# Kernel tuning notes

Measured on AMD Instinct MI355X. Metric: run time of the kernel, lower is better.

Reference implementation:

```python
import jax, jax.numpy as jnp
import numpy as np

H, KVH, HD = 32, 8, 128
DM = 4096
LN_L, LN_R = 64, 64
K_BITS, V_BITS = 4, 4
ROPE_THETA = 10000.0


def _rope(x, pos):
    # x: [B, nH, S, D], pos: [B, S]
    D = x.shape[-1]
    inv_freq = 1.0 / (ROPE_THETA ** (jnp.arange(0, D, 2, dtype=jnp.float32) / D))
    freqs = pos[:, :, None].astype(jnp.float32) * inv_freq            # [B,S,D/2]
    emb = jnp.concatenate([freqs, freqs], axis=-1)                     # [B,S,D]
    cos = jnp.cos(emb)[:, None, :, :]
    sin = jnp.sin(emb)[:, None, :, :]
    x1, x2 = x[..., : D // 2], x[..., D // 2:]
    rot = jnp.concatenate([-x2, x1], axis=-1)
    return x * cos + rot * sin


def _fake_quant(x, bits):
    # per-token (last-dim row) symmetric fake quantization
    qmax = 2.0 ** (bits - 1) - 1.0
    s = jnp.maximum(jnp.max(jnp.abs(x), axis=-1, keepdims=True) / qmax, 1e-8)
    return jnp.clip(jnp.round(x / s), -qmax, qmax) * s


def setup_inputs() -> dict:
    key = jax.random.key(0)
    ks = jax.random.split(key, 10)
    B, S = 1, 2048
    hidden_states = jax.random.normal(ks[0], (B, S, DM), dtype=jnp.float32)
    causal = jnp.tril(jnp.ones((S, S), dtype=bool))
    attention_mask = jnp.where(causal, 0.0, -1e9).astype(jnp.float32)[None, None]  # [1,1,S,S]
    position_ids = jnp.arange(S, dtype=jnp.int32)[None, :]
    sc = 1.0 / np.sqrt(DM)
    Wq = jax.random.normal(ks[1], (DM, H * HD), dtype=jnp.float32) * sc
    Wk = jax.random.normal(ks[2], (DM, KVH * HD), dtype=jnp.float32) * sc
    Wv = jax.random.normal(ks[3], (DM, KVH * HD), dtype=jnp.float32) * sc
    Wo = jax.random.normal(ks[4], (H * HD, DM), dtype=jnp.float32) * (1.0 / np.sqrt(H * HD))
    ln_left = jnp.eye(LN_L, dtype=jnp.float32) + 0.02 * jax.random.normal(ks[5], (LN_L, LN_L), dtype=jnp.float32)
    ln_right = jnp.eye(LN_R, dtype=jnp.float32) + 0.02 * jax.random.normal(ks[6], (LN_R, LN_R), dtype=jnp.float32)
    Tk = jnp.eye(HD, dtype=jnp.float32) + 0.05 * jax.random.normal(ks[7], (HD, HD), dtype=jnp.float32)
    Tv = jnp.eye(HD, dtype=jnp.float32) + 0.05 * jax.random.normal(ks[8], (HD, HD), dtype=jnp.float32)
    return {"hidden_states": hidden_states, "attention_mask": attention_mask,
            "position_ids": position_ids, "ln_left": ln_left, "ln_right": ln_right,
            "Wq": Wq, "Wk": Wk, "Wv": Wv, "Wo": Wo, "Tk": Tk, "Tv": Tv}


def reference(hidden_states, attention_mask, position_ids,
              ln_left, ln_right, Wq, Wk, Wv, Wo, Tk, Tv):
    B, S, _ = hidden_states.shape
    # ln_trans: Kronecker-decomposed SVD transform on hidden dim (64x64)
    h = hidden_states.reshape(B, S, LN_L, LN_R)
    h = jnp.einsum('bslr,la,rc->bsac', h, ln_left, ln_right).reshape(B, S, DM)
    # q/k/v projections (effective, trans-absorbed weights)
    q = (h @ Wq).reshape(B, S, H, HD).transpose(0, 2, 1, 3)    # [B,H,S,hd]
    k = (h @ Wk).reshape(B, S, KVH, HD).transpose(0, 2, 1, 3)  # [B,KVH,S,hd]
    v = ((h @ Wv).reshape(B, S, KVH, HD) @ Tv).transpose(0, 2, 1, 3)  # vcache_trans on V
    # RoPE
    q = _rope(q, position_ids)
    k = _rope(k, position_ids)
    # kcache_trans: q gets inv-transpose, k gets forward transform, then fake-quant K
    Tk_inv_t = jnp.linalg.inv(Tk).T
    q = q @ Tk_inv_t
    k = _fake_quant(k @ Tk, K_BITS)
    # vcache quant
    v = _fake_quant(v, V_BITS)
    # GQA repeat
    rep = H // KVH
    k = jnp.repeat(k, rep, axis=1)
    v = jnp.repeat(v, rep, axis=1)
    scores = jnp.einsum('bhqd,bhkd->bhqk', q, k) / np.sqrt(HD) + attention_mask
    p = jax.nn.softmax(scores.astype(jnp.float32), axis=-1).astype(q.dtype)
    o = jnp.einsum('bhqk,bhkd->bhqd', p, v).transpose(0, 2, 1, 3)  # [B,S,H,hd]
    # undo vcache_trans per head, then output projection
    o = o @ jnp.linalg.inv(Tv)
    return o.reshape(B, S, DM) @ Wo
```

## Files before the change

kernel.cpp:

```cpp
#include <hip/hip_runtime.h>
#include <math.h>

#define S_    2048
#define DM_   4096
#define H_    32
#define KVH_  8
#define HD_   128

typedef __bf16 bf16x8 __attribute__((ext_vector_type(8)));
typedef float  f32x4  __attribute__((ext_vector_type(4)));
typedef unsigned short u16x8 __attribute__((ext_vector_type(8)));
typedef unsigned short ushort_t;

__device__ __forceinline__ ushort_t f2b(float f) {
  unsigned int u = __float_as_uint(f);
  unsigned int r = (u + 0x7fffu + ((u >> 16) & 1u)) >> 16;
  return (ushort_t)r;
}
__device__ __forceinline__ float b2f(ushort_t h) {
  return __uint_as_float(((unsigned int)h) << 16);
}
__device__ __forceinline__ bf16x8 asbf(u16x8 v) {
  return __builtin_bit_cast(bf16x8, v);
}

__device__ __forceinline__ void gload16(const void* g, void* l) {
  __builtin_amdgcn_global_load_lds(
      (const __attribute__((address_space(1))) void*)g,
      (__attribute__((address_space(3))) void*)(unsigned int)(unsigned long long)l,
      16, 0, 0);
}

__global__ void newton_init(const float* __restrict__ A0, const float* __restrict__ A1,
                            float* __restrict__ X0, float* __restrict__ X1)
{
  const float* A = blockIdx.x ? A1 : A0;
  float*       X = blockIdx.x ? X1 : X0;
  const int i = blockIdx.y * 1024 + threadIdx.x;
  const int r = i >> 7, c = i & 127;
  X[i] = ((r == c) ? 2.0f : 0.0f) - A[i];
}

__global__ __launch_bounds__(256) void nmm(
    const float* __restrict__ A0, const float* __restrict__ B0, float* __restrict__ C0, int tr0,
    const float* __restrict__ A1, const float* __restrict__ B1, float* __restrict__ C1, int tr1,
    int update)
{
  const float* A = blockIdx.y ? A1 : A0;
  const float* B = blockIdx.y ? B1 : B0;
  float*       C = blockIdx.y ? C1 : C0;
  const int tr   = blockIdx.y ? tr1 : tr0;
  const int m0   = blockIdx.x * 32;
  const int tid  = threadIdx.x;

  __shared__ float Bs[128][132];
  __shared__ float As[32][132];

#pragma unroll
  for (int i = 0; i < 16; ++i) {
    int idx = tid + i * 256;
    int row = idx >> 5, c4 = (idx & 31) * 4;
    *(float4*)&Bs[row][c4] = *(const float4*)&B[row * 128 + c4];
  }
#pragma unroll
  for (int i = 0; i < 4; ++i) {
    int idx = tid + i * 256;
    int row = idx >> 5, c4 = (idx & 31) * 4;
    *(float4*)&As[row][c4] = *(const float4*)&A[(m0 + row) * 128 + c4];
  }
  __syncthreads();

  const int rloc = tid >> 3;
  const int c0   = (tid & 7) * 16;
  float acc[16];
#pragma unroll
  for (int j = 0; j < 16; ++j) acc[j] = 0.0f;
  for (int k = 0; k < 128; ++k) {
    float a = As[rloc][k];
#pragma unroll
    for (int j = 0; j < 16; j += 4) {
      float4 bv = *(const float4*)&Bs[k][c0 + j];
      acc[j + 0] += a * bv.x; acc[j + 1] += a * bv.y;
      acc[j + 2] += a * bv.z; acc[j + 3] += a * bv.w;
    }
  }
#pragma unroll
  for (int j = 0; j < 16; ++j) {
    float v = update ? (2.0f * As[rloc][c0 + j] - acc[j]) : acc[j];
    if (tr) C[(c0 + j) * 128 + (m0 + rloc)] = v;
    else    C[(m0 + rloc) * 128 + c0 + j]   = v;
  }
}

__global__ void prep_all(const float* __restrict__ Tkit, const float* __restrict__ Tk,
                         const float* __restrict__ Tv,   const float* __restrict__ TvI,
                         const float* __restrict__ lnR,  const float* __restrict__ lnL,
                         ushort_t* __restrict__ Fhi, ushort_t* __restrict__ Flo,
                         ushort_t* __restrict__ RBh, ushort_t* __restrict__ RBl,
                         ushort_t* __restrict__ LBh, ushort_t* __restrict__ LBl)
{
  const int mat = blockIdx.x;
  const int t   = threadIdx.x;
  if (mat < 4) {
    const float* src = (mat == 0) ? Tkit : ((mat == 1) ? Tk : ((mat == 2) ? Tv : TvI));
    const int tr = (mat == 3);
    ushort_t* hi = Fhi + mat * 16384;
    ushort_t* lo = Flo + mat * 16384;
    for (int ch = 0; ch < 32; ++ch) {
      int nt = ch >> 2, ds = ch & 3;
#pragma unroll
      for (int i = 0; i < 2; ++i) {
        int idx = t + i * 256;
        int ln = idx >> 3, j = idx & 7;
        int cc = ln & 15, gg = ln >> 4;
        int d = ds * 32 + gg * 8 + j, n = nt * 16 + cc;
        float x = tr ? src[n * 128 + d] : src[d * 128 + n];
        ushort_t hb = f2b(x);
        hi[(ch << 9) + idx] = hb;
        lo[(ch << 9) + idx] = f2b(x - b2f(hb));
      }
    }
  } else {
    const float* src = (mat == 4) ? lnR : lnL;
    ushort_t* hp = (mat == 4) ? RBh : LBh;
    ushort_t* lp = (mat == 4) ? RBl : LBl;
    for (int ch = 0; ch < 8; ++ch) {
      int nt = ch >> 1, ds = ch & 1;
#pragma unroll
      for (int i = 0; i < 2; ++i) {
        int idx = t + i * 256;
        int ln = idx >> 3, j = idx & 7;
        int cc = ln & 15, gg = ln >> 4;
        float x = src[(ds * 32 + gg * 8 + j) * 64 + nt * 16 + cc];
        ushort_t hb = f2b(x);
        hp[(ch << 9) + idx] = hb;
        lp[(ch << 9) + idx] = f2b(x - b2f(hb));
      }
    }
  }
}

__global__ void rope_table(const int* __restrict__ pos,
                           float* __restrict__ cosT, float* __restrict__ sinT)
{
  const int s = blockIdx.x, i = threadIdx.x;
  float invf = 1.0f / (float)pow(10000.0, (double)i * (1.0 / 64.0));
  float ang  = (float)pos[s] * invf;
  cosT[s * 64 + i] = cosf(ang);
  sinT[s * 64 + i] = sinf(ang);
}

__global__ __launch_bounds__(256) void ln3(
    const float* __restrict__ hid,
    const ushort_t* __restrict__ RBh, const ushort_t* __restrict__ RBl,
    const ushort_t* __restrict__ LBh, const ushort_t* __restrict__ LBl,
    ushort_t* __restrict__ hb16, ushort_t* __restrict__ hlo16)
{
  const int blk = blockIdx.x;
  const int tid = threadIdx.x;
  const int w = tid >> 6, lane = tid & 63;
  const int c = lane & 15, g = lane >> 4;

  __shared__ float Hs[4][64 * 68];

#pragma unroll
  for (int i = 0; i < 16; ++i) {
    int idx = tid + i * 256;
    int t = idx >> 10, e = idx & 1023;
    int l = e >> 4, r4 = (e & 15) * 4;
    *(float4*)&Hs[t][l * 68 + r4] =
        *(const float4*)&hid[((size_t)(blk * 4 + t)) * 4096 + l * 64 + r4];
  }
  __syncthreads();

  float* Hw = Hs[w];

  u16x8 ah[4][2], al[4][2];
#pragma unroll
  for (int mt = 0; mt < 4; ++mt)
#pragma unroll
    for (int ds = 0; ds < 2; ++ds) {
      u16x8 th, tl;
#pragma unroll
      for (int j = 0; j < 8; ++j) {
        float x = Hw[(mt * 16 + c) * 68 + ds * 32 + g * 8 + j];
        ushort_t hb = f2b(x); th[j] = hb; tl[j] = f2b(x - b2f(hb));
      }
      ah[mt][ds] = th; al[mt][ds] = tl;
    }

  f32x4 acc[4][4];
#pragma unroll
  for (int mt = 0; mt < 4; ++mt)
#pragma unroll
    for (int nt = 0; nt < 4; ++nt) acc[mt][nt] = (f32x4){0.f, 0.f, 0.f, 0.f};
#pragma unroll
  for (int nt = 0; nt < 4; ++nt) {
    u16x8 bh[2], bl[2];
#pragma unroll
    for (int ds = 0; ds < 2; ++ds) {
      bh[ds] = *(const u16x8*)(RBh + ((nt * 2 + ds) << 9) + lane * 8);
      bl[ds] = *(const u16x8*)(RBl + ((nt * 2 + ds) << 9) + lane * 8);
    }
#pragma unroll
    for (int mt = 0; mt < 4; ++mt)
#pragma unroll
      for (int ds = 0; ds < 2; ++ds) {
        acc[mt][nt] = __builtin_amdgcn_mfma_f32_16x16x32_bf16(asbf(ah[mt][ds]), asbf(bh[ds]), acc[mt][nt], 0, 0, 0);
        acc[mt][nt] = __builtin_amdgcn_mfma_f32_16x16x32_bf16(asbf(ah[mt][ds]), asbf(bl[ds]), acc[mt][nt], 0, 0, 0);
        acc[mt][nt] = __builtin_amdgcn_mfma_f32_16x16x32_bf16(asbf(al[mt][ds]), asbf(bh[ds]), acc[mt][nt], 0, 0, 0);
      }
  }

#pragma unroll
  for (int mt = 0; mt < 4; ++mt)
#pragma unroll
    for (int nt = 0; nt < 4; ++nt)
#pragma unroll
      for (int reg = 0; reg < 4; ++reg)
        Hw[(mt * 16 + g * 4 + reg) * 68 + nt * 16 + c] = acc[mt][nt][reg];

  u16x8 a2h[4][2], a2l[4][2];
#pragma unroll
  for (int mt = 0; mt < 4; ++mt)
#pragma unroll
    for (int ds = 0; ds < 2; ++ds) {
      a2h[mt][ds] = *(const u16x8*)(LBh + ((mt * 2 + ds) << 9) + lane * 8);
      a2l[mt][ds] = *(const u16x8*)(LBl + ((mt * 2 + ds) << 9) + lane * 8);
    }
  f32x4 acc2[4][4];
#pragma unroll
  for (int mt = 0; mt < 4; ++mt)
#pragma unroll
    for (int nt = 0; nt < 4; ++nt) acc2[mt][nt] = (f32x4){0.f, 0.f, 0.f, 0.f};
#pragma unroll
  for (int nt = 0; nt < 4; ++nt) {
#pragma unroll
    for (int ds = 0; ds < 2; ++ds) {
      u16x8 bh, bl;
#pragma unroll
      for (int j = 0; j < 8; ++j) {
        float x = Hw[(ds * 32 + g * 8 + j) * 68 + nt * 16 + c];
        ushort_t hb = f2b(x); bh[j] = hb; bl[j] = f2b(x - b2f(hb));
      }
#pragma unroll
      for (int mt = 0; mt < 4; ++mt) {
        acc2[mt][nt] = __builtin_amdgcn_mfma_f32_16x16x32_bf16(asbf(a2h[mt][ds]), asbf(bh), acc2[mt][nt], 0, 0, 0);
        acc2[mt][nt] = __builtin_amdgcn_mfma_f32_16x16x32_bf16(asbf(a2h[mt][ds]), asbf(bl), acc2[mt][nt], 0, 0, 0);
        acc2[mt][nt] = __builtin_amdgcn_mfma_f32_16x16x32_bf16(asbf(a2l[mt][ds]), asbf(bh), acc2[mt][nt], 0, 0, 0);
      }
    }
  }

  ushort_t* hp = (ushort_t*)Hw;
#pragma unroll
  for (int mt = 0; mt < 4; ++mt)
#pragma unroll
    for (int nt = 0; nt < 4; ++nt)
#pragma unroll
      for (int reg = 0; reg < 4; ++reg) {
        int a = mt * 16 + g * 4 + reg, cc2 = nt * 16 + c;
        float v = acc2[mt][nt][reg];
        ushort_t hb = f2b(v);
        hp[a * 64 + cc2] = hb;
        hp[4096 + a * 64 + cc2] = f2b(v - b2f(hb));
      }

  const size_t sbase = ((size_t)(blk * 4 + w)) * 4096;
#pragma unroll
  for (int i = 0; i < 8; ++i) {
    int idx = i * 64 + lane;
    int row = idx >> 3, c8 = (idx & 7) * 8;
    *(u16x8*)&hb16[sbase + row * 64 + c8]  = *(const u16x8*)&hp[row * 64 + c8];
    *(u16x8*)&hlo16[sbase + row * 64 + c8] = *(const u16x8*)&hp[4096 + row * 64 + c8];
  }
}

__global__ void wtrans(const float* __restrict__ W, ushort_t* __restrict__ WT,
                       int K, int N)
{
  __shared__ ushort_t t[64][68];
  const int tid = threadIdx.x;
  const int n0 = blockIdx.x * 64, k0 = blockIdx.y * 64;
  for (int idx = tid; idx < 4096; idx += 256) {
    int rr = idx >> 6, cc = idx & 63;
    t[cc][rr] = f2b(W[(size_t)(k0 + rr) * N + n0 + cc]);
  }
  __syncthreads();
  for (int idx = tid; idx < 4096; idx += 256) {
    int rr = idx >> 6, cc = idx & 63;
    WT[(size_t)(n0 + rr) * K + k0 + cc] = t[rr][cc];
  }
}

__global__ void wtrans_hl2(const float* __restrict__ Wk, const float* __restrict__ Wv,
                           ushort_t* __restrict__ WThi, ushort_t* __restrict__ WTlo)
{
  const int which = blockIdx.z;
  const float* W = which ? Wv : Wk;
  const int rowoff = which ? 1024 : 0;
  const int K = DM_, N = 1024;
  __shared__ ushort_t th[64][68];
  __shared__ ushort_t tl[64][68];
  const int tid = threadIdx.x;
  const int n0 = blockIdx.x * 64, k0 = blockIdx.y * 64;
  for (int idx = tid; idx < 4096; idx += 256) {
    int rr = idx >> 6, cc = idx & 63;
    float x = W[(size_t)(k0 + rr) * N + n0 + cc];
    ushort_t h = f2b(x);
    th[cc][rr] = h;
    tl[cc][rr] = f2b(x - b2f(h));
  }
  __syncthreads();
  for (int idx = tid; idx < 4096; idx += 256) {
    int rr = idx >> 6, cc = idx & 63;
    size_t o = (size_t)(rowoff + n0 + rr) * K + k0 + cc;
    WThi[o] = th[rr][cc];
    WTlo[o] = tl[rr][cc];
  }
}

__global__ __launch_bounds__(256) void wfold3(
    const float* __restrict__ Wo,
    const ushort_t* __restrict__ TBh, const ushort_t* __restrict__ TBl,
    ushort_t* __restrict__ WT)
{
  const int n0 = blockIdx.x * 128;
  const int h  = blockIdx.y;
  const int tid = threadIdx.x;
  const int w = tid >> 6, lane = tid & 63;
  const int c = lane & 15, g = lane >> 4;

  __shared__ float WoS[128 * 132];

#pragma unroll
  for (int i = 0; i < 16; ++i) {
    int idx = tid + i * 256;
    int e = idx >> 5, n4 = (idx & 31) * 4;
    *(float4*)&WoS[e * 132 + n4] =
        *(const float4*)&Wo[(size_t)(h * 128 + e) * 4096 + n0 + n4];
  }
  __syncthreads();

  u16x8 ah[2][4], al[2][4];
#pragma unroll
  for (int mt = 0; mt < 2; ++mt)
#pragma unroll
    for (int ds = 0; ds < 4; ++ds) {
      u16x8 th, tl;
#pragma unroll
      for (int j = 0; j < 8; ++j) {
        float x = WoS[(ds * 32 + g * 8 + j) * 132 + w * 32 + mt * 16 + c];
        ushort_t hb = f2b(x); th[j] = hb; tl[j] = f2b(x - b2f(hb));
      }
      ah[mt][ds] = th; al[mt][ds] = tl;
    }

  f32x4 acc[2][8];
#pragma unroll
  for (int mt = 0; mt < 2; ++mt)
#pragma unroll
    for (int nt = 0; nt < 8; ++nt) acc[mt][nt] = (f32x4){0.f, 0.f, 0.f, 0.f};
#pragma unroll
  for (int nt = 0; nt < 8; ++nt) {
#pragma unroll
    for (int ds = 0; ds < 4; ++ds) {
      u16x8 bh = *(const u16x8*)(TBh + ((nt * 4 + ds) << 9) + lane * 8);
      u16x8 bl = *(const u16x8*)(TBl + ((nt * 4 + ds) << 9) + lane * 8);
#pragma unroll
      for (int mt = 0; mt < 2; ++mt) {
        acc[mt][nt] = __builtin_amdgcn_mfma_f32_16x16x32_bf16(asbf(ah[mt][ds]), asbf(bh), acc[mt][nt], 0, 0, 0);
        acc[mt][nt] = __builtin_amdgcn_mfma_f32_16x16x32_bf16(asbf(ah[mt][ds]), asbf(bl), acc[mt][nt], 0, 0, 0);
        acc[mt][nt] = __builtin_amdgcn_mfma_f32_16x16x32_bf16(asbf(al[mt][ds]), asbf(bh), acc[mt][nt], 0, 0, 0);
      }
    }
  }
  __syncthreads();

  ushort_t* OS = (ushort_t*)WoS;
#pragma unroll
  for (int mt = 0; mt < 2; ++mt)
#pragma unroll
    for (int nt = 0; nt < 8; ++nt)
#pragma unroll
      for (int reg = 0; reg < 4; ++reg)
        OS[(w * 32 + mt * 16 + g * 4 + reg) * 136 + nt * 16 + c] = f2b(acc[mt][nt][reg]);
  __syncthreads();

#pragma unroll
  for (int i = 0; i < 8; ++i) {
    int idx = tid + i * 256;
    int nn = idx >> 4, c8 = (idx & 15) * 8;
    *(u16x8*)&WT[(size_t)(n0 + nn) * 4096 + h * 128 + c8] = *(const u16x8*)&OS[nn * 136 + c8];
  }
}

__global__ __launch_bounds__(256) void gemm_bf16(const ushort_t* __restrict__ A,
                                                 const ushort_t* __restrict__ BT,
                                                 float* __restrict__ C,
                                                 int M, int N, int K, int qlayout)
{
  __shared__ __align__(16) ushort_t As[128 * 64];
  __shared__ __align__(16) ushort_t Bs[128 * 64];
  const int tid = threadIdx.x;
  const int bm = blockIdx.y * 128, bn = blockIdx.x * 128;
  const int lane = tid & 63, w = tid >> 6;
  const int c = lane & 15, g = lane >> 4;
  const int wm = (w >> 1) * 64, wn = (w & 1) * 64;
  f32x4 acc[4][4];
#pragma unroll
  for (int mt = 0; mt < 4; ++mt)
#pragma unroll
    for (int nt = 0; nt < 4; ++nt) acc[mt][nt] = (f32x4){0.f, 0.f, 0.f, 0.f};
  const int srow = tid >> 3;
  const int slot = (tid & 7) ^ (srow & 7);
  for (int k0 = 0; k0 < K; k0 += 64) {
    __syncthreads();
#pragma unroll
    for (int ii = 0; ii < 4; ++ii) {
      gload16(A  + (size_t)(bm + ii * 32 + srow) * K + k0 + slot * 8,
              (char*)As + w * 1024 + ii * 4096);
      gload16(BT + (size_t)(bn + ii * 32 + srow) * K + k0 + slot * 8,
              (char*)Bs + w * 1024 + ii * 4096);
    }
    __syncthreads();
#pragma unroll
    for (int ks = 0; ks < 2; ++ks) {
      bf16x8 av[4], bv[4];
#pragma unroll
      for (int mt = 0; mt < 4; ++mt)
        av[mt] = *(const bf16x8*)((const char*)As + (wm + mt * 16 + c) * 128 +
                                  (((ks * 4 + g) ^ (c & 7)) << 4));
#pragma unroll
      for (int nt = 0; nt < 4; ++nt)
        bv[nt] = *(const bf16x8*)((const char*)Bs + (wn + nt * 16 + c) * 128 +
                                  (((ks * 4 + g) ^ (c & 7)) << 4));
#pragma unroll
      for (int mt = 0; mt < 4; ++mt)
#pragma unroll
        for (int nt = 0; nt < 4; ++nt)
          acc[mt][nt] = __builtin_amdgcn_mfma_f32_16x16x32_bf16(av[mt], bv[nt], acc[mt][nt], 0, 0, 0);
    }
  }
#pragma unroll
  for (int mt = 0; mt < 4; ++mt)
#pragma unroll
    for (int nt = 0; nt < 4; ++nt)
#pragma unroll
      for (int reg = 0; reg < 4; ++reg) {
        int m = bm + wm + mt * 16 + g * 4 + reg;
        int n = bn + wn + nt * 16 + c;
        float v = acc[mt][nt][reg];
        if (qlayout) C[((size_t)(n >> 7) * S_ + m) * 128 + (n & 127)] = v;
        else         C[(size_t)m * N + n] = v;
      }
}

__global__ __launch_bounds__(256) void gemm_bf16_3(
    const ushort_t* __restrict__ Ahi, const ushort_t* __restrict__ Alo,
    const ushort_t* __restrict__ BThi, const ushort_t* __restrict__ BTlo,
    float* __restrict__ Ck, float* __restrict__ Cv, int M, int N, int K)
{
  __shared__ __align__(16) ushort_t Ash[128 * 64];
  __shared__ __align__(16) ushort_t Asl[128 * 64];
  __shared__ __align__(16) ushort_t Bsh[64 * 64];
  __shared__ __align__(16) ushort_t Bsl[64 * 64];
  const int tid = threadIdx.x;
  const int bm = blockIdx.y * 128, bn = blockIdx.x * 64;
  const int lane = tid & 63, w = tid >> 6;
  const int c = lane & 15, g = lane >> 4;
  const int wm = w * 32;
  f32x4 acc[2][4];
#pragma unroll
  for (int mt = 0; mt < 2; ++mt)
#pragma unroll
    for (int nt = 0; nt < 4; ++nt) acc[mt][nt] = (f32x4){0.f, 0.f, 0.f, 0.f};
  const int srow = tid >> 3;
  const int slot = (tid & 7) ^ (srow & 7);
  for (int k0 = 0; k0 < K; k0 += 64) {
    __syncthreads();
#pragma unroll
    for (int ii = 0; ii < 4; ++ii) {
      const size_t ga = (size_t)(bm + ii * 32 + srow) * K + k0 + slot * 8;
      gload16(Ahi + ga, (char*)Ash + w * 1024 + ii * 4096);
      gload16(Alo + ga, (char*)Asl + w * 1024 + ii * 4096);
    }
#pragma unroll
    for (int ii = 0; ii < 2; ++ii) {
      const size_t gb = (size_t)(bn + ii * 32 + srow) * K + k0 + slot * 8;
      gload16(BThi + gb, (char*)Bsh + w * 1024 + ii * 4096);
      gload16(BTlo + gb, (char*)Bsl + w * 1024 + ii * 4096);
    }
    __syncthreads();
#pragma unroll
    for (int ks = 0; ks < 2; ++ks) {
      bf16x8 ah[2], al[2], bh[4], bl[4];
#pragma unroll
      for (int mt = 0; mt < 2; ++mt) {
        int ro = (wm + mt * 16 + c) * 128;
        int so = ((ks * 4 + g) ^ (c & 7)) << 4;
        ah[mt] = *(const bf16x8*)((const char*)Ash + ro + so);
        al[mt] = *(const bf16x8*)((const char*)Asl + ro + so);
      }
#pragma unroll
      for (int nt = 0; nt < 4; ++nt) {
        int ro = (nt * 16 + c) * 128;
        int so = ((ks * 4 + g) ^ (c & 7)) << 4;
        bh[nt] = *(const bf16x8*)((const char*)Bsh + ro + so);
        bl[nt] = *(const bf16x8*)((const char*)Bsl + ro + so);
      }
#pragma unroll
      for (int mt = 0; mt < 2; ++mt)
#pragma unroll
        for (int nt = 0; nt < 4; ++nt) {
          acc[mt][nt] = __builtin_amdgcn_mfma_f32_16x16x32_bf16(ah[mt], bh[nt], acc[mt][nt], 0, 0, 0);
          acc[mt][nt] = __builtin_amdgcn_mfma_f32_16x16x32_bf16(ah[mt], bl[nt], acc[mt][nt], 0, 0, 0);
          acc[mt][nt] = __builtin_amdgcn_mfma_f32_16x16x32_bf16(al[mt], bh[nt], acc[mt][nt], 0, 0, 0);
        }
    }
  }
#pragma unroll
  for (int mt = 0; mt < 2; ++mt)
#pragma unroll
    for (int nt = 0; nt < 4; ++nt)
#pragma unroll
      for (int reg = 0; reg < 4; ++reg) {
        int m = bm + wm + mt * 16 + g * 4 + reg;
        int n = bn + nt * 16 + c;
        float v = acc[mt][nt][reg];
        if (n < 1024) Ck[((size_t)(n >> 7) * S_ + m) * 128 + (n & 127)] = v;
        else          Cv[((size_t)((n - 1024) >> 7) * S_ + m) * 128 + (n & 127)] = v;
      }
}

__global__ __launch_bounds__(256) void tpost_all(
    const float* __restrict__ qsrc, const float* __restrict__ ksrc,
    const float* __restrict__ vsrc,
    const ushort_t* __restrict__ tfH, const ushort_t* __restrict__ tfL,
    const float* __restrict__ cosT, const float* __restrict__ sinT,
    ushort_t* __restrict__ qfrag, ushort_t* __restrict__ kfrag,
    ushort_t* __restrict__ vfrag)
{
  const int b = blockIdx.x;
  const float* src; const ushort_t *Thi, *Tlo; ushort_t* outp; int mode, blk;
  if (b < 2048)      { src = qsrc; Thi = tfH;             Tlo = tfL;             outp = qfrag; mode = 0; blk = b; }
  else if (b < 2560) { src = ksrc; Thi = tfH + 16384;     Tlo = tfL + 16384;     outp = kfrag; mode = 1; blk = b - 2048; }
  else               { src = vsrc; Thi = tfH + 2 * 16384; Tlo = tfL + 2 * 16384; outp = vfrag; mode = 2; blk = b - 2560; }

  const int tid = threadIdx.x;
  const int w = tid >> 6, lane = tid & 63;
  const int c = lane & 15, g = lane >> 4;

  __shared__ float raw_[32 * 132];
  __shared__ float rop_[32 * 132];
  __shared__ __align__(16) ushort_t vtile[32][136];

#pragma unroll
  for (int i = 0; i < 4; ++i) {
    int idx = tid + i * 256;
    int row = idx >> 5, c4 = (idx & 31) * 4;
    *(float4*)&raw_[row * 132 + c4] =
        *(const float4*)&src[(size_t)(blk * 32 + row) * 128 + c4];
  }
  __syncthreads();

  {
    const int r = tid >> 3, co = (tid & 7) * 16;
    if (mode <= 1) {
      const int s = (blk & 63) * 32 + r;
      const float* ct = cosT + (size_t)s * 64;
      const float* st = sinT + (size_t)s * 64;
#pragma unroll
      for (int j = 0; j < 16; ++j) {
        int cc = co + j, i2 = cc & 63;
        float x = raw_[r * 132 + cc];
        float other = (cc < 64) ? raw_[r * 132 + cc + 64] : raw_[r * 132 + cc - 64];
        rop_[r * 132 + cc] = (cc < 64) ? (x * ct[i2] - other * st[i2])
                                       : (x * ct[i2] + other * st[i2]);
      }
    } else {
#pragma unroll
      for (int j = 0; j < 16; ++j) {
        int cc = co + j;
        rop_[r * 132 + cc] = raw_[r * 132 + cc];
      }
    }
  }
  __syncthreads();

  u16x8 ahu[2][4], alu[2][4];
#pragma unroll
  for (int mt = 0; mt < 2; ++mt)
#pragma unroll
    for (int ds = 0; ds < 4; ++ds) {
      u16x8 th, tl;
#pragma unroll
      for (int j = 0; j < 8; ++j) {
        float x = rop_[(mt * 16 + c) * 132 + ds * 32 + g * 8 + j];
        ushort_t hb = f2b(x);
        th[j] = hb;
        tl[j] = f2b(x - b2f(hb));
      }
      ahu[mt][ds] = th;
      alu[mt][ds] = tl;
    }

  f32x4 acc[2][2];
#pragma unroll
  for (int mt = 0; mt < 2; ++mt)
#pragma unroll
    for (int nl = 0; nl < 2; ++nl) acc[mt][nl] = (f32x4){0.f, 0.f, 0.f, 0.f};
#pragma unroll
  for (int nl = 0; nl < 2; ++nl) {
    const int nt = w * 2 + nl;
    u16x8 bh[4], bl[4];
#pragma unroll
    for (int ds = 0; ds < 4; ++ds) {
      bh[ds] = *(const u16x8*)(Thi + ((nt * 4 + ds) << 9) + lane * 8);
      bl[ds] = *(const u16x8*)(Tlo + ((nt * 4 + ds) << 9) + lane * 8);
    }
#pragma unroll
    for (int mt = 0; mt < 2; ++mt)
#pragma unroll
      for (int ds = 0; ds < 4; ++ds) {
        acc[mt][nl] = __builtin_amdgcn_mfma_f32_16x16x32_bf16(asbf(ahu[mt][ds]), asbf(bh[ds]), acc[mt][nl], 0, 0, 0);
        acc[mt][nl] = __builtin_amdgcn_mfma_f32_16x16x32_bf16(asbf(ahu[mt][ds]), asbf(bl[ds]), acc[mt][nl], 0, 0, 0);
        acc[mt][nl] = __builtin_amdgcn_mfma_f32_16x16x32_bf16(asbf(alu[mt][ds]), asbf(bh[ds]), acc[mt][nl], 0, 0, 0);
      }
  }
  __syncthreads();

#pragma unroll
  for (int mt = 0; mt < 2; ++mt)
#pragma unroll
    for (int nl = 0; nl < 2; ++nl)
#pragma unroll
      for (int reg = 0; reg < 4; ++reg)
        raw_[(mt * 16 + g * 4 + reg) * 132 + (w * 2 + nl) * 16 + c] = acc[mt][nl][reg];
  __syncthreads();

  const int r = tid >> 3, co = (tid & 7) * 16;
  float vals[16];
#pragma unroll
  for (int j = 0; j < 16; ++j) vals[j] = raw_[r * 132 + co + j];

  if (mode == 0) {
#pragma unroll
    for (int j = 0; j < 16; ++j) vals[j] *= 0.08838834764831845f;
  } else {
    float m = 0.0f;
#pragma unroll
    for (int j = 0; j < 16; ++j) m = fmaxf(m, fabsf(vals[j]));
    m = fmaxf(m, __shfl_xor(m, 1));
    m = fmaxf(m, __shfl_xor(m, 2));
    m = fmaxf(m, __shfl_xor(m, 4));
    const float sc = fmaxf(m * (1.0f / 7.0f), 1e-8f);
#pragma unroll
    for (int j = 0; j < 16; ++j) {
      float qv = rintf(vals[j] / sc);
      qv = fminf(7.0f, fmaxf(-7.0f, qv));
      vals[j] = qv * sc;
    }
  }

  if (mode <= 1) {
    const size_t chunkbase = ((size_t)blk << 13) +
                             ((size_t)((r >> 4) * 4 + (co >> 5)) << 10);
    const int lane0 = ((co >> 3) & 3) * 16 + (r & 15);
    const int lane1 = (((co + 8) >> 3) & 3) * 16 + (r & 15);
    u16x8 o0, o1;
#pragma unroll
    for (int j = 0; j < 8; ++j) { o0[j] = f2b(vals[j]); o1[j] = f2b(vals[j + 8]); }
    *(u16x8*)((char*)outp + chunkbase + lane0 * 16) = o0;
    *(u16x8*)((char*)outp + chunkbase + lane1 * 16) = o1;
  } else {
#pragma unroll
    for (int j = 0; j < 16; ++j) vtile[r][co + j] = f2b(vals[j]);
    __syncthreads();
#pragma unroll
    for (int i = 0; i < 2; ++i) {
      int id = tid + i * 256;
      int dt = id >> 6, ln = id & 63;
      int gg = ln >> 4, cc = ln & 15;
      u16x8 o;
#pragma unroll
      for (int j = 0; j < 8; ++j) o[j] = vtile[gg * 8 + j][dt * 16 + cc];
      *(u16x8*)(outp + (((size_t)blk) << 12) + (dt << 9) + ln * 8) = o;
    }
  }
}

__global__ __launch_bounds__(256) void attn_mfma6(
    const ushort_t* __restrict__ qf_,
    const ushort_t* __restrict__ kf_,
    const ushort_t* __restrict__ vf_,
    ushort_t* __restrict__ o16)
{
  const int lid = blockIdx.x;
  const int xcd = lid & 7;
  const int idx = lid >> 3;
  const int h   = xcd * 4 + (idx & 3);
  const int kb  = idx >> 2;
  const int kvh = xcd;

  const int tid = threadIdx.x;
  const int w    = tid >> 6;
  const int lane = tid & 63;
  const int c = lane & 15, g = lane >> 4;
  const int qt = (w < 2) ? (2 * kb + w) : (60 - 2 * kb + w);

  __shared__ __align__(16) ushort_t Ps[4][2][16][40];

  const float LOG2E = 1.44269504f;
  const float MBIAS = 28.8539008f;

  const char* qtile = (const char*)qf_ + (((size_t)(h * 64 + qt)) << 13);
  bf16x8 qf[2][4];
#pragma unroll
  for (int mt = 0; mt < 2; ++mt)
#pragma unroll
    for (int ds = 0; ds < 4; ++ds)
      qf[mt][ds] = *(const bf16x8*)(qtile + ((mt * 4 + ds) << 10) + lane * 16);

  bf16x8 ones;
#pragma unroll
  for (int j = 0; j < 8; ++j) ones[j] = (__bf16)1.0f;

  f32x4 oa[2][8];
#pragma unroll
  for (int mt = 0; mt < 2; ++mt)
#pragma unroll
    for (int dt = 0; dt < 8; ++dt) oa[mt][dt] = (f32x4){0.f, 0.f, 0.f, 0.f};
  f32x4 la[2];
  la[0] = (f32x4){0.f, 0.f, 0.f, 0.f};
  la[1] = (f32x4){0.f, 0.f, 0.f, 0.f};

  const char* kbase = (const char*)kf_ + (((size_t)kvh * 64) << 13);
  const char* vbase = (const char*)vf_ + (((size_t)kvh * 64) << 13);

  for (int kt = 0; kt <= qt; ++kt) {
    const char* ktile = kbase + ((size_t)kt << 13);
    const char* vtile = vbase + ((size_t)kt << 13);
    bf16x8 kc[2][4], vc[8];
#pragma unroll
    for (int nt = 0; nt < 2; ++nt)
#pragma unroll
      for (int ds = 0; ds < 4; ++ds)
        kc[nt][ds] = *(const bf16x8*)(ktile + ((nt * 4 + ds) << 10) + lane * 16);
#pragma unroll
    for (int dt = 0; dt < 8; ++dt)
      vc[dt] = *(const bf16x8*)(vtile + (dt << 10) + lane * 16);

    f32x4 sc[2][2];
#pragma unroll
    for (int mt = 0; mt < 2; ++mt)
#pragma unroll
      for (int nt = 0; nt < 2; ++nt) sc[mt][nt] = (f32x4){0.f, 0.f, 0.f, 0.f};
    __builtin_amdgcn_s_setprio(1);
#pragma unroll
    for (int ds = 0; ds < 4; ++ds) {
      sc[0][0] = __builtin_amdgcn_mfma_f32_16x16x32_bf16(qf[0][ds], kc[0][ds], sc[0][0], 0, 0, 0);
      sc[0][1] = __builtin_amdgcn_mfma_f32_16x16x32_bf16(qf[0][ds], kc[1][ds], sc[0][1], 0, 0, 0);
      sc[1][0] = __builtin_amdgcn_mfma_f32_16x16x32_bf16(qf[1][ds], kc[0][ds], sc[1][0], 0, 0, 0);
      sc[1][1] = __builtin_amdgcn_mfma_f32_16x16x32_bf16(qf[1][ds], kc[1][ds], sc[1][1], 0, 0, 0);
    }
    __builtin_amdgcn_s_setprio(0);

#pragma unroll
    for (int mt = 0; mt < 2; ++mt) {
#pragma unroll
      for (int reg = 0; reg < 4; ++reg) {
        float s0 = sc[mt][0][reg], s1 = sc[mt][1][reg];
        if (kt == qt) {
          int qrl = mt * 16 + g * 4 + reg;
          if (c > qrl)      s0 = -INFINITY;
          if (16 + c > qrl) s1 = -INFINITY;
        }
        float p0 = exp2f(s0 * LOG2E - MBIAS);
        float p1 = exp2f(s1 * LOG2E - MBIAS);
        Ps[w][mt][g * 4 + reg][c]      = f2b(p0);
        Ps[w][mt][g * 4 + reg][16 + c] = f2b(p1);
      }
    }

    bf16x8 pa0 = *reinterpret_cast<const bf16x8*>(&Ps[w][0][c][g * 8]);
    bf16x8 pa1 = *reinterpret_cast<const bf16x8*>(&Ps[w][1][c][g * 8]);
    __builtin_amdgcn_s_setprio(1);
#pragma unroll
    for (int dt = 0; dt < 8; ++dt) {
      oa[0][dt] = __builtin_amdgcn_mfma_f32_16x16x32_bf16(pa0, vc[dt], oa[0][dt], 0, 0, 0);
      oa[1][dt] = __builtin_amdgcn_mfma_f32_16x16x32_bf16(pa1, vc[dt], oa[1][dt], 0, 0, 0);
    }
    la[0] = __builtin_amdgcn_mfma_f32_16x16x32_bf16(pa0, ones, la[0], 0, 0, 0);
    la[1] = __builtin_amdgcn_mfma_f32_16x16x32_bf16(pa1, ones, la[1], 0, 0, 0);
    __builtin_amdgcn_s_setprio(0);
  }

#pragma unroll
  for (int mt = 0; mt < 2; ++mt)
#pragma unroll
    for (int reg = 0; reg < 4; ++reg) {
      float li = 1.0f / la[mt][reg];
      int srow = qt * 32 + mt * 16 + g * 4 + reg;
      ushort_t* orow = o16 + (size_t)srow * DM_ + h * 128;
#pragma unroll
      for (int dt = 0; dt < 8; ++dt)
        orow[dt * 16 + c] = f2b(oa[mt][dt][reg] * li);
    }
}

extern "C" void kernel_launch(void* const* d_in, const int* in_sizes, int n_in,
                              void* d_out, int out_size, void* d_ws, size_t ws_size,
                              hipStream_t stream)
{
  (void)in_sizes; (void)n_in; (void)out_size; (void)ws_size;
  const float* hidden = (const float*)d_in[0];
  const int*   pos    = (const int*)d_in[2];
  const float* lnL    = (const float*)d_in[3];
  const float* lnR    = (const float*)d_in[4];
  const float* Wq     = (const float*)d_in[5];
  const float* Wk     = (const float*)d_in[6];
  const float* Wv     = (const float*)d_in[7];
  const float* Wo     = (const float*)d_in[8];
  const float* Tk     = (const float*)d_in[9];
  const float* Tv     = (const float*)d_in[10];
  float* out = (float*)d_out;

  float* ws   = (float*)d_ws;
  float* hbuf = ws;
  float* kbuf = hbuf + (size_t)S_ * DM_;
  float* vbuf = kbuf + (size_t)S_ * KVH_ * HD_;
  float* Tkit = vbuf + (size_t)S_ * KVH_ * HD_;
  float* TvI  = Tkit + 128 * 128;
  float* cosT = TvI + 128 * 128;
  float* sinT = cosT + (size_t)S_ * 64;
  ushort_t* hb16 = (ushort_t*)(sinT + (size_t)S_ * 64);
  ushort_t* WT   = hb16 + (size_t)S_ * DM_;
  float* nb      = (float*)(WT + (size_t)DM_ * DM_);
  ushort_t* tfH  = (ushort_t*)(nb + 6 * 16384);
  ushort_t* tfL  = tfH + 4 * 16384;
  ushort_t* RBh  = tfL + 4 * 16384;
  ushort_t* RBl  = RBh + 4096;
  ushort_t* LBh  = RBl + 4096;
  ushort_t* LBl  = LBh + 4096;

  char* hbytes = (char*)hbuf;
  ushort_t* hlo16 = (ushort_t*)hbytes;
  ushort_t* qfrag = (ushort_t*)hbytes;
  ushort_t* kfrag = (ushort_t*)(hbytes + (16u << 20));
  ushort_t* vfrag = (ushort_t*)(hbytes + (20u << 20));

  ushort_t* WTkh = WT;
  ushort_t* WTkl = WT + (size_t)2048 * DM_;

  float* Xk = nb,              *Xv = nb + 16384;
  float* Yk = nb + 2 * 16384,  *Yv = nb + 3 * 16384;
  float* Xk2 = nb + 4 * 16384, *Xv2 = nb + 5 * 16384;

  float* qbuf = out;

  newton_init<<<dim3(2, 16), 1024, 0, stream>>>(Tk, Tv, Xk, Xv);
  for (int it = 0; it < 4; ++it) {
    nmm<<<dim3(4, 2), 256, 0, stream>>>(Tk, Xk, Yk, 0, Tv, Xv, Yv, 0, 0);
    const int last = (it == 3);
    float* ok = last ? Tkit : Xk2;
    float* ov = last ? TvI  : Xv2;
    nmm<<<dim3(4, 2), 256, 0, stream>>>(Xk, Yk, ok, last ? 1 : 0, Xv, Yv, ov, 0, 1);
    float* t;
    t = Xk; Xk = Xk2; Xk2 = t;
    t = Xv; Xv = Xv2; Xv2 = t;
  }
  prep_all<<<6, 256, 0, stream>>>(Tkit, Tk, Tv, TvI, lnR, lnL,
                                  tfH, tfL, RBh, RBl, LBh, LBl);

  rope_table<<<S_, 64, 0, stream>>>(pos, cosT, sinT);
  ln3<<<S_ / 4, 256, 0, stream>>>(hidden, RBh, RBl, LBh, LBl, hb16, hlo16);

  wtrans<<<dim3(DM_ / 64, DM_ / 64), 256, 0, stream>>>(Wq, WT, DM_, DM_);
  gemm_bf16<<<dim3(DM_ / 128, S_ / 128), 256, 0, stream>>>(hb16, WT, qbuf, S_, DM_, DM_, 1);
  wtrans_hl2<<<dim3(16, 64, 2), 256, 0, stream>>>(Wk, Wv, WTkh, WTkl);
  gemm_bf16_3<<<dim3(32, S_ / 128), 256, 0, stream>>>(hb16, hlo16, WTkh, WTkl,
                                                      kbuf, vbuf, S_, 2048, DM_);

  tpost_all<<<3072, 256, 0, stream>>>(qbuf, kbuf, vbuf, tfH, tfL,
                                      cosT, sinT, qfrag, kfrag, vfrag);

  attn_mfma6<<<dim3(S_ / 128 * H_), 256, 0, stream>>>(qfrag, kfrag, vfrag, hb16);

  wfold3<<<dim3(DM_ / 128, H_), 256, 0, stream>>>(Wo, tfH + 3 * 16384, tfL + 3 * 16384, WT);
  gemm_bf16<<<dim3(DM_ / 128, S_ / 128), 256, 0, stream>>>(hb16, WT, out, S_, DM_, DM_, 0);
}
```

Before: 576.3 us.

## Merge QKV projection GEMMs, weight transposes and rope/LN prep into combined launches

Fuses the Wq transpose and the Wk/Wv hi/lo transpose into one kernel. It also merges the rope table into the LN kernel as extra blocks, and combines the Q GEMM and the split-precision KV GEMM into one launch whose blocks alternate between the two paths. The goal is to cut launch count and kernel-boundary idle time, and to let the two GEMMs share the GPU instead of each leaving tail gaps. In exchange it raises shared-memory use per block to the larger of the two paths, which may lower occupancy. It also places the transposed Wq in a new workspace region after LBl, which relies on the workspace being large enough.

```diff
diff --git a/kernel.cpp b/kernel.cpp
--- a/kernel.cpp
+++ b/kernel.cpp
@@ -140,28 +140,74 @@
   }
 }
 
-__global__ void rope_table(const int* __restrict__ pos,
-                           float* __restrict__ cosT, float* __restrict__ sinT)
-{
-  const int s = blockIdx.x, i = threadIdx.x;
-  float invf = 1.0f / (float)pow(10000.0, (double)i * (1.0 / 64.0));
-  float ang  = (float)pos[s] * invf;
-  cosT[s * 64 + i] = cosf(ang);
-  sinT[s * 64 + i] = sinf(ang);
-}
-
-__global__ __launch_bounds__(256) void ln3(
-    const float* __restrict__ hid,
+__global__ void trans_all(const float* __restrict__ Wq, const float* __restrict__ Wk,
+                          const float* __restrict__ Wv,
+                          ushort_t* __restrict__ WT,
+                          ushort_t* __restrict__ WThi, ushort_t* __restrict__ WTlo)
+{
+  const int b = blockIdx.x;
+  const int tid = threadIdx.x;
+  __shared__ ushort_t th[64][68];
+  __shared__ ushort_t tl[64][68];
+  if (b < 4096) {
+    const int n0 = (b & 63) * 64, k0 = (b >> 6) * 64;
+    for (int idx = tid; idx < 4096; idx += 256) {
+      int rr = idx >> 6, cc = idx & 63;
+      th[cc][rr] = f2b(Wq[(size_t)(k0 + rr) * DM_ + n0 + cc]);
+    }
+    __syncthreads();
+    for (int idx = tid; idx < 4096; idx += 256) {
+      int rr = idx >> 6, cc = idx & 63;
+      WT[(size_t)(n0 + rr) * DM_ + k0 + cc] = th[rr][cc];
+    }
+  } else {
+    const int b2 = b - 4096;
+    const int which = b2 >> 10;
+    const int b3 = b2 & 1023;
+    const float* W = which ? Wv : Wk;
+    const int rowoff = which ? 1024 : 0;
+    const int n0 = (b3 & 15) * 64, k0 = (b3 >> 4) * 64;
+    for (int idx = tid; idx < 4096; idx += 256) {
+      int rr = idx >> 6, cc = idx & 63;
+      float x = W[(size_t)(k0 + rr) * 1024 + n0 + cc];
+      ushort_t h = f2b(x);
+      th[cc][rr] = h;
+      tl[cc][rr] = f2b(x - b2f(h));
+    }
+    __syncthreads();
+    for (int idx = tid; idx < 4096; idx += 256) {
+      int rr = idx >> 6, cc = idx & 63;
+      size_t o = (size_t)(rowoff + n0 + rr) * DM_ + k0 + cc;
+      WThi[o] = th[rr][cc];
+      WTlo[o] = tl[rr][cc];
+    }
+  }
+}
+
+__global__ __launch_bounds__(256) void lnrope(
+    const float* __restrict__ hid, const int* __restrict__ pos,
     const ushort_t* __restrict__ RBh, const ushort_t* __restrict__ RBl,
     const ushort_t* __restrict__ LBh, const ushort_t* __restrict__ LBl,
-    ushort_t* __restrict__ hb16, ushort_t* __restrict__ hlo16)
-{
-  const int blk = blockIdx.x;
+    ushort_t* __restrict__ hb16, ushort_t* __restrict__ hlo16,
+    float* __restrict__ cosT, float* __restrict__ sinT)
+{
+  __shared__ float Hs[4][64 * 68];
+  const int bid = blockIdx.x;
   const int tid = threadIdx.x;
+
+  if (bid >= 512) {
+    const int s = (bid - 512) * 4 + (tid >> 6);
+    const int i = tid & 63;
+    float invf = 1.0f / (float)pow(10000.0, (double)i * (1.0 / 64.0));
+    float ang  = (float)pos[s] * invf;
+    cosT[s * 64 + i] = cosf(ang);
+    sinT[s * 64 + i] = sinf(ang);
+    return;
+  }
+
+  const int blk = bid;
   const int w = tid >> 6, lane = tid & 63;
   const int c = lane & 15, g = lane >> 4;
-
-  __shared__ float Hs[4][64 * 68];
 
 #pragma unroll
   for (int i = 0; i < 16; ++i) {
@@ -273,50 +319,6 @@
     int row = idx >> 3, c8 = (idx & 7) * 8;
     *(u16x8*)&hb16[sbase + row * 64 + c8]  = *(const u16x8*)&hp[row * 64 + c8];
     *(u16x8*)&hlo16[sbase + row * 64 + c8] = *(const u16x8*)&hp[4096 + row * 64 + c8];
-  }
-}
-
-__global__ void wtrans(const float* __restrict__ W, ushort_t* __restrict__ WT,
-                       int K, int N)
-{
-  __shared__ ushort_t t[64][68];
-  const int tid = threadIdx.x;
-  const int n0 = blockIdx.x * 64, k0 = blockIdx.y * 64;
-  for (int idx = tid; idx < 4096; idx += 256) {
-    int rr = idx >> 6, cc = idx & 63;
-    t[cc][rr] = f2b(W[(size_t)(k0 + rr) * N + n0 + cc]);
-  }
-  __syncthreads();
-  for (int idx = tid; idx < 4096; idx += 256) {
-    int rr = idx >> 6, cc = idx & 63;
-    WT[(size_t)(n0 + rr) * K + k0 + cc] = t[rr][cc];
-  }
-}
-
-__global__ void wtrans_hl2(const float* __restrict__ Wk, const float* __restrict__ Wv,
-                           ushort_t* __restrict__ WThi, ushort_t* __restrict__ WTlo)
-{
-  const int which = blockIdx.z;
-  const float* W = which ? Wv : Wk;
-  const int rowoff = which ? 1024 : 0;
-  const int K = DM_, N = 1024;
-  __shared__ ushort_t th[64][68];
-  __shared__ ushort_t tl[64][68];
-  const int tid = threadIdx.x;
-  const int n0 = blockIdx.x * 64, k0 = blockIdx.y * 64;
-  for (int idx = tid; idx < 4096; idx += 256) {
-    int rr = idx >> 6, cc = idx & 63;
-    float x = W[(size_t)(k0 + rr) * N + n0 + cc];
-    ushort_t h = f2b(x);
-    th[cc][rr] = h;
-    tl[cc][rr] = f2b(x - b2f(h));
-  }
-  __syncthreads();
-  for (int idx = tid; idx < 4096; idx += 256) {
-    int rr = idx >> 6, cc = idx & 63;
-    size_t o = (size_t)(rowoff + n0 + rr) * K + k0 + cc;
-    WThi[o] = th[rr][cc];
-    WTlo[o] = tl[rr][cc];
   }
 }
 
@@ -456,81 +458,138 @@
       }
 }
 
-__global__ __launch_bounds__(256) void gemm_bf16_3(
+__global__ __launch_bounds__(256) void gemm_qkv(
     const ushort_t* __restrict__ Ahi, const ushort_t* __restrict__ Alo,
-    const ushort_t* __restrict__ BThi, const ushort_t* __restrict__ BTlo,
-    float* __restrict__ Ck, float* __restrict__ Cv, int M, int N, int K)
-{
-  __shared__ __align__(16) ushort_t Ash[128 * 64];
-  __shared__ __align__(16) ushort_t Asl[128 * 64];
-  __shared__ __align__(16) ushort_t Bsh[64 * 64];
-  __shared__ __align__(16) ushort_t Bsl[64 * 64];
+    const ushort_t* __restrict__ WqT,
+    const ushort_t* __restrict__ KVh, const ushort_t* __restrict__ KVl,
+    float* __restrict__ Cq, float* __restrict__ Ck, float* __restrict__ Cv)
+{
+  __shared__ __align__(16) char smem[49152];
+  const int b = blockIdx.x;
+  const int path = b & 1;
+  const int idx = b >> 1;
   const int tid = threadIdx.x;
-  const int bm = blockIdx.y * 128, bn = blockIdx.x * 64;
   const int lane = tid & 63, w = tid >> 6;
   const int c = lane & 15, g = lane >> 4;
-  const int wm = w * 32;
-  f32x4 acc[2][4];
-#pragma unroll
-  for (int mt = 0; mt < 2; ++mt)
-#pragma unroll
-    for (int nt = 0; nt < 4; ++nt) acc[mt][nt] = (f32x4){0.f, 0.f, 0.f, 0.f};
   const int srow = tid >> 3;
   const int slot = (tid & 7) ^ (srow & 7);
-  for (int k0 = 0; k0 < K; k0 += 64) {
-    __syncthreads();
-#pragma unroll
-    for (int ii = 0; ii < 4; ++ii) {
-      const size_t ga = (size_t)(bm + ii * 32 + srow) * K + k0 + slot * 8;
-      gload16(Ahi + ga, (char*)Ash + w * 1024 + ii * 4096);
-      gload16(Alo + ga, (char*)Asl + w * 1024 + ii * 4096);
-    }
-#pragma unroll
-    for (int ii = 0; ii < 2; ++ii) {
-      const size_t gb = (size_t)(bn + ii * 32 + srow) * K + k0 + slot * 8;
-      gload16(BThi + gb, (char*)Bsh + w * 1024 + ii * 4096);
-      gload16(BTlo + gb, (char*)Bsl + w * 1024 + ii * 4096);
-    }
-    __syncthreads();
-#pragma unroll
-    for (int ks = 0; ks < 2; ++ks) {
-      bf16x8 ah[2], al[2], bh[4], bl[4];
-#pragma unroll
-      for (int mt = 0; mt < 2; ++mt) {
-        int ro = (wm + mt * 16 + c) * 128;
-        int so = ((ks * 4 + g) ^ (c & 7)) << 4;
-        ah[mt] = *(const bf16x8*)((const char*)Ash + ro + so);
-        al[mt] = *(const bf16x8*)((const char*)Asl + ro + so);
-      }
-#pragma unroll
-      for (int nt = 0; nt < 4; ++nt) {
-        int ro = (nt * 16 + c) * 128;
-        int so = ((ks * 4 + g) ^ (c & 7)) << 4;
-        bh[nt] = *(const bf16x8*)((const char*)Bsh + ro + so);
-        bl[nt] = *(const bf16x8*)((const char*)Bsl + ro + so);
-      }
-#pragma unroll
-      for (int mt = 0; mt < 2; ++mt)
+  const int K = DM_;
+
+  if (path == 0) {
+    ushort_t* As = (ushort_t*)smem;
+    ushort_t* Bs = (ushort_t*)smem + 128 * 64;
+    const int bn = (idx & 31) * 128, bm = (idx >> 5) * 128;
+    const int wm = (w >> 1) * 64, wn = (w & 1) * 64;
+    f32x4 acc[4][4];
+#pragma unroll
+    for (int mt = 0; mt < 4; ++mt)
+#pragma unroll
+      for (int nt = 0; nt < 4; ++nt) acc[mt][nt] = (f32x4){0.f, 0.f, 0.f, 0.f};
+    for (int k0 = 0; k0 < K; k0 += 64) {
+      __syncthreads();
+#pragma unroll
+      for (int ii = 0; ii < 4; ++ii) {
+        gload16(Ahi + (size_t)(bm + ii * 32 + srow) * K + k0 + slot * 8,
+                (char*)As + w * 1024 + ii * 4096);
+        gload16(WqT + (size_t)(bn + ii * 32 + srow) * K + k0 + slot * 8,
+                (char*)Bs + w * 1024 + ii * 4096);
+      }
+      __syncthreads();
+#pragma unroll
+      for (int ks = 0; ks < 2; ++ks) {
+        bf16x8 av[4], bv[4];
+#pragma unroll
+        for (int mt = 0; mt < 4; ++mt)
+          av[mt] = *(const bf16x8*)((const char*)As + (wm + mt * 16 + c) * 128 +
+                                    (((ks * 4 + g) ^ (c & 7)) << 4));
+#pragma unroll
+        for (int nt = 0; nt < 4; ++nt)
+          bv[nt] = *(const bf16x8*)((const char*)Bs + (wn + nt * 16 + c) * 128 +
+                                    (((ks * 4 + g) ^ (c & 7)) << 4));
+#pragma unroll
+        for (int mt = 0; mt < 4; ++mt)
+#pragma unroll
+          for (int nt = 0; nt < 4; ++nt)
+            acc[mt][nt] = __builtin_amdgcn_mfma_f32_16x16x32_bf16(av[mt], bv[nt], acc[mt][nt], 0, 0, 0);
+      }
+    }
+#pragma unroll
+    for (int mt = 0; mt < 4; ++mt)
+#pragma unroll
+      for (int nt = 0; nt < 4; ++nt)
+#pragma unroll
+        for (int reg = 0; reg < 4; ++reg) {
+          int m = bm + wm + mt * 16 + g * 4 + reg;
+          int n = bn + wn + nt * 16 + c;
+          Cq[((size_t)(n >> 7) * S_ + m) * 128 + (n & 127)] = acc[mt][nt][reg];
+        }
+  } else {
+    ushort_t* Ash = (ushort_t*)smem;
+    ushort_t* Asl = Ash + 128 * 64;
+    ushort_t* Bsh = Asl + 128 * 64;
+    ushort_t* Bsl = Bsh + 64 * 64;
+    const int bn = (idx & 31) * 64, bm = (idx >> 5) * 128;
+    const int wm = w * 32;
+    f32x4 acc[2][4];
+#pragma unroll
+    for (int mt = 0; mt < 2; ++mt)
+#pragma unroll
+      for (int nt = 0; nt < 4; ++nt) acc[mt][nt] = (f32x4){0.f, 0.f, 0.f, 0.f};
+    for (int k0 = 0; k0 < K; k0 += 64) {
+      __syncthreads();
+#pragma unroll
+      for (int ii = 0; ii < 4; ++ii) {
+        const size_t ga = (size_t)(bm + ii * 32 + srow) * K + k0 + slot * 8;
+        gload16(Ahi + ga, (char*)Ash + w * 1024 + ii * 4096);
+        gload16(Alo + ga, (char*)Asl + w * 1024 + ii * 4096);
+      }
+#pragma unroll
+      for (int ii = 0; ii < 2; ++ii) {
+        const size_t gb = (size_t)(bn + ii * 32 + srow) * K + k0 + slot * 8;
+        gload16(KVh + gb, (char*)Bsh + w * 1024 + ii * 4096);
+        gload16(KVl + gb, (char*)Bsl + w * 1024 + ii * 4096);
+      }
+      __syncthreads();
+#pragma unroll
+      for (int ks = 0; ks < 2; ++ks) {
+        bf16x8 ah[2], al[2], bh[4], bl[4];
+#pragma unroll
+        for (int mt = 0; mt < 2; ++mt) {
+          int ro = (wm + mt * 16 + c) * 128;
+          int so = ((ks * 4 + g) ^ (c & 7)) << 4;
+          ah[mt] = *(const bf16x8*)((const char*)Ash + ro + so);
+          al[mt] = *(const bf16x8*)((const char*)Asl + ro + so);
+        }
 #pragma unroll
         for (int nt = 0; nt < 4; ++nt) {
-          acc[mt][nt] = __builtin_amdgcn_mfma_f32_16x16x32_bf16(ah[mt], bh[nt], acc[mt][nt], 0, 0, 0);
-          acc[mt][nt] = __builtin_amdgcn_mfma_f32_16x16x32_bf16(ah[mt], bl[nt], acc[mt][nt], 0, 0, 0);
-          acc[mt][nt] = __builtin_amdgcn_mfma_f32_16x16x32_bf16(al[mt], bh[nt], acc[mt][nt], 0, 0, 0);
+          int ro = (nt * 16 + c) * 128;
+          int so = ((ks * 4 + g) ^ (c & 7)) << 4;
+          bh[nt] = *(const bf16x8*)((const char*)Bsh + ro + so);
+          bl[nt] = *(const bf16x8*)((const char*)Bsl + ro + so);
         }
-    }
-  }
-#pragma unroll
-  for (int mt = 0; mt < 2; ++mt)
-#pragma unroll
-    for (int nt = 0; nt < 4; ++nt)
-#pragma unroll
-      for (int reg = 0; reg < 4; ++reg) {
-        int m = bm + wm + mt * 16 + g * 4 + reg;
-        int n = bn + nt * 16 + c;
-        float v = acc[mt][nt][reg];
-        if (n < 1024) Ck[((size_t)(n >> 7) * S_ + m) * 128 + (n & 127)] = v;
-        else          Cv[((size_t)((n - 1024) >> 7) * S_ + m) * 128 + (n & 127)] = v;
-      }
+#pragma unroll
+        for (int mt = 0; mt < 2; ++mt)
+#pragma unroll
+          for (int nt = 0; nt < 4; ++nt) {
+            acc[mt][nt] = __builtin_amdgcn_mfma_f32_16x16x32_bf16(ah[mt], bh[nt], acc[mt][nt], 0, 0, 0);
+            acc[mt][nt] = __builtin_amdgcn_mfma_f32_16x16x32_bf16(ah[mt], bl[nt], acc[mt][nt], 0, 0, 0);
+            acc[mt][nt] = __builtin_amdgcn_mfma_f32_16x16x32_bf16(al[mt], bh[nt], acc[mt][nt], 0, 0, 0);
+          }
+      }
+    }
+#pragma unroll
+    for (int mt = 0; mt < 2; ++mt)
+#pragma unroll
+      for (int nt = 0; nt < 4; ++nt)
+#pragma unroll
+        for (int reg = 0; reg < 4; ++reg) {
+          int m = bm + wm + mt * 16 + g * 4 + reg;
+          int n = bn + nt * 16 + c;
+          float v = acc[mt][nt][reg];
+          if (n < 1024) Ck[((size_t)(n >> 7) * S_ + m) * 128 + (n & 127)] = v;
+          else          Cv[((size_t)((n - 1024) >> 7) * S_ + m) * 128 + (n & 127)] = v;
+        }
+  }
 }
 
 __global__ __launch_bounds__(256) void tpost_all(
@@ -852,6 +911,8 @@
 
   ushort_t* WTkh = WT;
   ushort_t* WTkl = WT + (size_t)2048 * DM_;
+  ushort_t* WqT  = WT + (size_t)2048 * DM_ * 2;
+  ushort_t* WqTbuf = LBl + 4096;
 
   float* Xk = nb,              *Xv = nb + 16384;
   float* Yk = nb + 2 * 16384,  *Yv = nb + 3 * 16384;
@@ -873,14 +934,12 @@
   prep_all<<<6, 256, 0, stream>>>(Tkit, Tk, Tv, TvI, lnR, lnL,
                                   tfH, tfL, RBh, RBl, LBh, LBl);
 
-  rope_table<<<S_, 64, 0, stream>>>(pos, cosT, sinT);
-  ln3<<<S_ / 4, 256, 0, stream>>>(hidden, RBh, RBl, LBh, LBl, hb16, hlo16);
-
-  wtrans<<<dim3(DM_ / 64, DM_ / 64), 256, 0, stream>>>(Wq, WT, DM_, DM_);
-  gemm_bf16<<<dim3(DM_ / 128, S_ / 128), 256, 0, stream>>>(hb16, WT, qbuf, S_, DM_, DM_, 1);
-  wtrans_hl2<<<dim3(16, 64, 2), 256, 0, stream>>>(Wk, Wv, WTkh, WTkl);
-  gemm_bf16_3<<<dim3(32, S_ / 128), 256, 0, stream>>>(hb16, hlo16, WTkh, WTkl,
-                                                      kbuf, vbuf, S_, 2048, DM_);
+  trans_all<<<6144, 256, 0, stream>>>(Wq, Wk, Wv, WqTbuf, WTkh, WTkl);
+  lnrope<<<1024, 256, 0, stream>>>(hidden, pos, RBh, RBl, LBh, LBl,
+                                   hb16, hlo16, cosT, sinT);
+
+  gemm_qkv<<<1024, 256, 0, stream>>>(hb16, hlo16, WqTbuf, WTkh, WTkl,
+                                     qbuf, kbuf, vbuf);
 
   tpost_all<<<3072, 256, 0, stream>>>(qbuf, kbuf, vbuf, tfH, tfL,
                                       cosT, sinT, qfrag, kfrag, vfrag);
```

New measurement: 568.2 us, median of 2. No clear change (-1.4%).
